# Performance work log

Measured on AMD Instinct MI355X. Metric: run time of the kernel, lower is better.

The kernel has to match this reference:

```python
import jax, jax.numpy as jnp
import numpy as np

B, S, D = 4, 2048, 1024
H, DK = 16, 64
NUM_BUCKETS = 32
MAX_DISTANCE = 128
EPS = 1e-6


def _relative_position_bucket(q_len, kv_len):
    # causal (bidirectional=False) T5 bucketization
    ctx = jnp.arange(q_len, dtype=jnp.int32)[:, None]
    mem = jnp.arange(kv_len, dtype=jnp.int32)[None, :]
    rp = mem - ctx                       # [q, kv]
    rp = -jnp.minimum(rp, 0)             # nonnegative distances to the past
    max_exact = NUM_BUCKETS // 2
    is_small = rp < max_exact
    rp_safe = jnp.maximum(rp, 1).astype(jnp.float32)
    large = max_exact + (
        jnp.log(rp_safe / max_exact) / np.log(MAX_DISTANCE / max_exact) * (NUM_BUCKETS - max_exact)
    ).astype(jnp.int32)
    large = jnp.minimum(large, NUM_BUCKETS - 1)
    return jnp.where(is_small, rp, large)  # [q, kv] int32 in [0, NUM_BUCKETS)


def setup_inputs() -> dict:
    key = jax.random.key(0)
    k1, k2, k3, k4 = jax.random.split(key, 4)
    hidden_states = jax.random.normal(k1, (B, S, D), dtype=jnp.float32)
    sequence_mask = jnp.ones((B, S), dtype=bool)
    rms_w = jnp.ones((D,), dtype=jnp.float32)
    W_qkv = jax.random.normal(k2, (D, 3 * H * DK), dtype=jnp.float32) * (D ** -0.5)
    W_o = jax.random.normal(k3, (H * DK, D), dtype=jnp.float32) * ((H * DK) ** -0.5)
    rel_bias = jax.random.normal(k4, (NUM_BUCKETS, H), dtype=jnp.float32)
    return {"hidden_states": hidden_states, "sequence_mask": sequence_mask,
            "rms_w": rms_w, "W_qkv": W_qkv, "W_o": W_o, "rel_bias": rel_bias}


def reference(hidden_states, sequence_mask, rms_w, W_qkv, W_o, rel_bias):
    # RMSNorm
    var = jnp.mean(hidden_states * hidden_states, axis=-1, keepdims=True)
    normed = hidden_states * jax.lax.rsqrt(var + EPS) * rms_w

    # QKV projection -> [B, S, 3, H, DK] -> [B, H, S, DK] each
    qkv = (normed @ W_qkv).reshape(B, S, 3, H, DK)
    q = jnp.transpose(qkv[:, :, 0], (0, 2, 1, 3))
    k = jnp.transpose(qkv[:, :, 1], (0, 2, 1, 3))
    v = jnp.transpose(qkv[:, :, 2], (0, 2, 1, 3))

    # relative position bias: gather [S,S,H] -> [1,H,S,S]
    bucket = _relative_position_bucket(S, S)
    pos_bias = jnp.transpose(rel_bias[bucket], (2, 0, 1))[None]

    # scores (note: T5 does NOT scale by 1/sqrt(dk))
    scores = jnp.einsum("bhqd,bhkd->bhqk", q, k) + pos_bias

    # causal mask combined with sequence mask (True = attend)
    causal = jnp.tril(jnp.ones((S, S), dtype=bool))
    mask = causal[None, None] & sequence_mask[:, None, None, :]
    scores = jnp.where(mask, scores, jnp.finfo(scores.dtype).min)

    attn = jax.nn.softmax(scores.astype(jnp.float32), axis=-1).astype(scores.dtype)
    # dropout p=0 / eval mode -> identity
    ctx = jnp.einsum("bhqk,bhkd->bhqd", attn, v)          # [B,H,S,DK]
    ctx = jnp.transpose(ctx, (0, 2, 1, 3)).reshape(B, S, H * DK)
    out = hidden_states + ctx @ W_o                        # residual
    return out
```

## Files before the change

kernel.cpp:

```cpp
#include <hip/hip_runtime.h>
#include <math.h>


typedef unsigned short ushort_t;
typedef __attribute__((ext_vector_type(8))) short bfrag;
typedef __attribute__((ext_vector_type(4))) float ffrag;

#define MFMA16(a, b, c) __builtin_amdgcn_mfma_f32_16x16x32_bf16((a), (b), (c), 0, 0, 0)
#define LOG2E 1.4426950408889634f

__device__ __forceinline__ void load_lds16(const ushort_t* g, ushort_t* l) {
  __builtin_amdgcn_global_load_lds(
      (const __attribute__((address_space(1))) unsigned int*)g,
      (__attribute__((address_space(3))) unsigned int*)l, 16, 0, 0);
}

__device__ __forceinline__ ushort_t f2bf(float f) {
  union { float f; unsigned u; } x; x.f = f;
  unsigned r = x.u + 0x7FFFu + ((x.u >> 16) & 1u);
  return (ushort_t)(r >> 16);
}
__device__ __forceinline__ float bf2f(ushort_t u) {
  union { unsigned u; float f; } x; x.u = ((unsigned)u) << 16; return x.f;
}
__device__ __forceinline__ unsigned cvtpk(float lo, float hi) {
  unsigned r;
  asm("v_cvt_pk_bf16_f32 %0, %1, %2" : "=v"(r) : "v"(lo), "v"(hi));
  return r;
}
__device__ __forceinline__ float exp2fast(float x) {
  return __builtin_amdgcn_exp2f(x);
}

__global__ __launch_bounds__(256) void norm_cvt_kernel(
    const float* __restrict__ hidden, const float* __restrict__ rms_w,
    ushort_t* __restrict__ normed) {
  const int w = threadIdx.x >> 6, lane = threadIdx.x & 63;
  const int row = blockIdx.x * 4 + w;
  const float* p = hidden + (size_t)row * 1024;
  float4 v[4];
  float s = 0.f;
#pragma unroll
  for (int i = 0; i < 4; ++i) {
    v[i] = *(const float4*)(p + (lane + i * 64) * 4);
    s += v[i].x * v[i].x + v[i].y * v[i].y + v[i].z * v[i].z + v[i].w * v[i].w;
  }
#pragma unroll
  for (int off = 1; off < 64; off <<= 1) s += __shfl_xor(s, off, 64);
  const float scale = rsqrtf(s * (1.0f / 1024.0f) + 1e-6f);
#pragma unroll
  for (int i = 0; i < 4; ++i) {
    const int c0 = (lane + i * 64) * 4;
    float4 wv = *(const float4*)(rms_w + c0);
    ushort4 u;
    u.x = f2bf(v[i].x * scale * wv.x);
    u.y = f2bf(v[i].y * scale * wv.y);
    u.z = f2bf(v[i].z * scale * wv.z);
    u.w = f2bf(v[i].w * scale * wv.w);
    *(ushort4*)(normed + (size_t)row * 1024 + c0) = u;
  }
}

__global__ __launch_bounds__(256) void transpose_cvt_kernel(
    const float* __restrict__ in, ushort_t* __restrict__ out, int R, int C) {
  __shared__ float tile[32][33];
  const int r0 = blockIdx.y * 32, c0 = blockIdx.x * 32;
  const int tr = threadIdx.x >> 5, tc = threadIdx.x & 31;
#pragma unroll
  for (int i = 0; i < 32; i += 8)
    tile[tr + i][tc] = in[(size_t)(r0 + tr + i) * C + c0 + tc];
  __syncthreads();
#pragma unroll
  for (int i = 0; i < 32; i += 8)
    out[(size_t)(c0 + tr + i) * R + r0 + tc] = f2bf(tile[tc][tr + i]);
}

__global__ __launch_bounds__(256, 2) void qkv_mfma_kernel(
    const ushort_t* __restrict__ A, const ushort_t* __restrict__ Bt,
    ushort_t* __restrict__ qbf, ushort_t* __restrict__ kbf,
    ushort_t* __restrict__ vtbf) {
  __shared__ ushort_t As[2][128][64];
  __shared__ ushort_t Bs[2][128][64];
  const int tid = threadIdx.x, lane = tid & 63, w = tid >> 6;
  const int quad = lane >> 4, ln = lane & 15;
  const int wr = w >> 1, wc = w & 1;
  const int id = blockIdx.x;
  const int xcd = id & 7, t8 = id >> 3;
  const int by = xcd * 8 + t8 / 24, bx = t8 % 24;
  const int m0 = by * 128, n0 = bx * 128;
  const int rswz = ln & 7;

  auto stage = [&](const ushort_t* src, ushort_t* lds, int gr0, int gc0) {
#pragma unroll
    for (int i = 0; i < 4; ++i) {
      const int idx = i * 256 + tid;
      const int r = idx >> 3, c = idx & 7;
      load_lds16(src + (size_t)(gr0 + r) * 1024 + gc0 + ((c ^ (r & 7)) * 8),
                 lds + idx * 8);
    }
  };

  ffrag acc[4][4];
#pragma unroll
  for (int i = 0; i < 4; ++i)
#pragma unroll
    for (int j = 0; j < 4; ++j) acc[i][j] = (ffrag)0.f;

  stage(A, &As[0][0][0], m0, 0);
  stage(Bt, &Bs[0][0][0], n0, 0);
  asm volatile("s_waitcnt vmcnt(0)" ::: "memory");
  __builtin_amdgcn_s_barrier();

  for (int t = 0; t < 16; ++t) {
    const int cur = t & 1;
    if (t + 1 < 16) {
      stage(A, &As[cur ^ 1][0][0], m0, (t + 1) * 64);
      stage(Bt, &Bs[cur ^ 1][0][0], n0, (t + 1) * 64);
    }
    bfrag a[4][2], b[4][2];
#pragma unroll
    for (int mi = 0; mi < 4; ++mi) {
      const int rA = wr * 64 + mi * 16 + ln;
#pragma unroll
      for (int ks = 0; ks < 2; ++ks)
        a[mi][ks] = *(const bfrag*)(&As[cur][rA][((ks * 4 + quad) ^ rswz) * 8]);
    }
#pragma unroll
    for (int ni = 0; ni < 4; ++ni) {
      const int rB = wc * 64 + ni * 16 + ln;
#pragma unroll
      for (int ks = 0; ks < 2; ++ks)
        b[ni][ks] = *(const bfrag*)(&Bs[cur][rB][((ks * 4 + quad) ^ rswz) * 8]);
    }
    __builtin_amdgcn_s_setprio(1);
#pragma unroll
    for (int mi = 0; mi < 4; ++mi)
#pragma unroll
      for (int ni = 0; ni < 4; ++ni)
#pragma unroll
        for (int ks = 0; ks < 2; ++ks)
          acc[mi][ni] = MFMA16(a[mi][ks], b[ni][ks], acc[mi][ni]);
    __builtin_amdgcn_s_setprio(0);
    asm volatile("s_waitcnt vmcnt(0)" ::: "memory");
    __builtin_amdgcn_s_barrier();
  }

  const int b_idx = m0 >> 11;
  const int cbase = n0 + wc * 64 + ln;
#pragma unroll
  for (int mi = 0; mi < 4; ++mi) {
    const int sbase = (m0 & 2047) + wr * 64 + mi * 16 + quad * 4;
#pragma unroll
    for (int ni = 0; ni < 4; ++ni) {
      const int c = cbase + ni * 16;
      const int three = c >> 10, rem = c & 1023;
      const int h = rem >> 6, dk = rem & 63;
      if (three == 2) {
        ushort4 u;
        u.x = f2bf(acc[mi][ni][0]); u.y = f2bf(acc[mi][ni][1]);
        u.z = f2bf(acc[mi][ni][2]); u.w = f2bf(acc[mi][ni][3]);
        *(ushort4*)(vtbf + ((size_t)(b_idx * 16 + h) * 64 + dk) * 2048 + sbase) = u;
      } else {
        const float sc = (three == 0) ? 1.0f : LOG2E;
        ushort_t* dst = (three == 0 ? qbf : kbf) +
                        ((size_t)(b_idx * 16 + h) * 2048 + sbase) * 64 + dk;
        dst[0]   = f2bf(acc[mi][ni][0] * sc);
        dst[64]  = f2bf(acc[mi][ni][1] * sc);
        dst[128] = f2bf(acc[mi][ni][2] * sc);
        dst[192] = f2bf(acc[mi][ni][3] * sc);
      }
    }
  }
}

__global__ __launch_bounds__(512, 6) void attn_mfma_kernel(
    const ushort_t* __restrict__ qbf, const ushort_t* __restrict__ kbf,
    const ushort_t* __restrict__ vtbf, const float* __restrict__ rel_bias,
    ushort_t* __restrict__ ctx) {
  __shared__ ushort_t Kt[2][2][64][32];
  __shared__ ushort_t Vt[2][2][64][32];
  __shared__ ushort_t Pt[128][64];
  __shared__ ushort_t bias_t[2048];

  const int tid = threadIdx.x, w = tid >> 6, lane = tid & 63;
  const int quad = lane >> 4, ln = lane & 15;
  const int id = blockIdx.x;
  const int bh = id & 63;
  const int qb = 15 - (id >> 6);
  const int h = bh & 15;
  const int nt = 2 * qb + 2;
  const int q0w = qb * 128 + w * 16;

  for (int dist = tid; dist < 2048; dist += 512) {
    int bucket;
    if (dist < 16) bucket = dist;
    else {
      bucket = 16 + (int)(logf((float)dist * (1.0f / 16.0f)) * (16.0f / logf(8.0f)));
      if (bucket > 31) bucket = 31;
    }
    bias_t[dist] = f2bf(rel_bias[bucket * 16 + h] * LOG2E);
  }
  const float c31 = bf2f(f2bf(rel_bias[31 * 16 + h] * LOG2E));
  __syncthreads();

  const size_t khead = (size_t)bh * 2048 * 64;
  const int skf = tid >> 8;
  const int srow = (tid >> 2) & 63;
  const int ssw = ((tid & 3) ^ ((srow >> 1) & 3)) * 8;
  const int rsw = ((ln >> 1) & 3) * 8;
  const int psw = (ln & 7) * 8;

  bfrag aq[2];
#pragma unroll
  for (int kf = 0; kf < 2; ++kf)
    aq[kf] = *(const bfrag*)(qbf + ((size_t)bh * 2048 + q0w + ln) * 64 +
                             kf * 32 + quad * 8);

  bfrag ones;
#pragma unroll
  for (int i = 0; i < 8; ++i) ones[i] = (short)0x3F80;

  ffrag o[4], l_acc;
#pragma unroll
  for (int nd = 0; nd < 4; ++nd) o[nd] = (ffrag)0.f;
  l_acc = (ffrag)0.f;
  float m_run = -3.0e38f;

  load_lds16(kbf + khead + (size_t)srow * 64 + skf * 32 + ssw,
             &Kt[0][0][0][0] + tid * 8);
  load_lds16(vtbf + khead + (size_t)srow * 2048 + 0 + skf * 32 + ssw,
             &Vt[0][0][0][0] + tid * 8);

  int cur = 0;
  for (int j = 0; j < nt; ++j) {
    const int key0 = j * 64;
    asm volatile("s_waitcnt vmcnt(0)" ::: "memory");
    __builtin_amdgcn_s_barrier();

    if (j + 1 < nt) {
      const int nk0 = key0 + 64;
      load_lds16(kbf + khead + (size_t)(nk0 + srow) * 64 + skf * 32 + ssw,
                 &Kt[cur ^ 1][0][0][0] + tid * 8);
      load_lds16(vtbf + khead + (size_t)srow * 2048 + nk0 + skf * 32 + ssw,
                 &Vt[cur ^ 1][0][0][0] + tid * 8);
    }

    if (key0 <= q0w + 15) {
      ffrag s[4];
#pragma unroll
      for (int mi = 0; mi < 4; ++mi) s[mi] = (ffrag)0.f;
      __builtin_amdgcn_s_setprio(1);
#pragma unroll
      for (int kf = 0; kf < 2; ++kf)
#pragma unroll
        for (int mi = 0; mi < 4; ++mi) {
          bfrag ak = *(const bfrag*)&Kt[cur][kf][mi * 16 + ln][(quad * 8) ^ rsw];
          s[mi] = MFMA16(ak, aq[kf], s[mi]);
        }
      __builtin_amdgcn_s_setprio(0);

      const bool diagT = (key0 + 63 > q0w);
      const bool fastT = (key0 + 176 <= q0w);
      float sbias = 0.f;
      if (fastT) {
        sbias = c31;
      } else if (diagT) {
        const int q = q0w + ln;
#pragma unroll
        for (int mi = 0; mi < 4; ++mi) {
          const int keyb = key0 + mi * 16 + quad * 4;
#pragma unroll
          for (int r = 0; r < 4; ++r) {
            const int dist = q - (keyb + r);
            const int db = dist < 0 ? 0 : dist;
            s[mi][r] = (dist < 0) ? -3.0e38f : (s[mi][r] + bf2f(bias_t[db]));
          }
        }
      } else {
        const int q = q0w + ln;
#pragma unroll
        for (int mi = 0; mi < 4; ++mi) {
          const int keyb = key0 + mi * 16 + quad * 4;
#pragma unroll
          for (int r = 0; r < 4; ++r)
            s[mi][r] += bf2f(bias_t[q - (keyb + r)]);
        }
      }

      float m0_ = fmaxf(fmaxf(s[0][0], s[0][1]), fmaxf(s[0][2], s[0][3]));
      float m1_ = fmaxf(fmaxf(s[1][0], s[1][1]), fmaxf(s[1][2], s[1][3]));
      float m2_ = fmaxf(fmaxf(s[2][0], s[2][1]), fmaxf(s[2][2], s[2][3]));
      float m3_ = fmaxf(fmaxf(s[3][0], s[3][1]), fmaxf(s[3][2], s[3][3]));
      const float mxl = fmaxf(fmaxf(m0_, m1_), fmaxf(m2_, m3_)) + sbias;

      if (!__all(mxl <= m_run + 8.0f)) {
        float mx = mxl;
        mx = fmaxf(mx, __shfl_xor(mx, 16, 64));
        mx = fmaxf(mx, __shfl_xor(mx, 32, 64));
        const float mnew = fmaxf(m_run, mx);
        const float alpha = exp2fast(m_run - mnew);
        m_run = mnew;
#pragma unroll
        for (int r = 0; r < 4; ++r) {
          const float af = __shfl(alpha, quad * 4 + r, 64);
#pragma unroll
          for (int nd = 0; nd < 4; ++nd) o[nd][r] *= af;
          l_acc[r] *= af;
        }
      }
      const float sh = m_run - sbias;
#pragma unroll
      for (int mi = 0; mi < 4; ++mi)
#pragma unroll
        for (int r = 0; r < 4; ++r)
          s[mi][r] = exp2fast(s[mi][r] - sh);

      {
        ushort_t* prow = &Pt[w * 16 + ln][0];
#pragma unroll
        for (int mi = 0; mi < 4; ++mi) {
          uint2 pk;
          pk.x = cvtpk(s[mi][0], s[mi][1]);
          pk.y = cvtpk(s[mi][2], s[mi][3]);
          *(uint2*)(prow + ((mi * 16 + quad * 4) ^ psw)) = pk;
        }
      }

      __builtin_amdgcn_s_setprio(1);
#pragma unroll
      for (int kf = 0; kf < 2; ++kf) {
        bfrag ap = *(const bfrag*)&Pt[w * 16 + ln][(kf * 32 + quad * 8) ^ psw];
        l_acc = MFMA16(ap, ones, l_acc);
#pragma unroll
        for (int nd = 0; nd < 4; ++nd) {
          bfrag bv = *(const bfrag*)&Vt[cur][kf][nd * 16 + ln][(quad * 8) ^ rsw];
          o[nd] = MFMA16(ap, bv, o[nd]);
        }
      }
      __builtin_amdgcn_s_setprio(0);
    }
    cur ^= 1;
  }

  ffrag inv;
#pragma unroll
  for (int r = 0; r < 4; ++r) inv[r] = 1.0f / l_acc[r];
  const int s0 = q0w + quad * 4;
#pragma unroll
  for (int nd = 0; nd < 4; ++nd)
#pragma unroll
    for (int r = 0; r < 4; ++r)
      ctx[((size_t)(bh >> 4) * 2048 + s0 + r) * 1024 + h * 64 + nd * 16 + ln] =
          f2bf(o[nd][r] * inv[r]);
}

__global__ __launch_bounds__(256, 2) void out_mfma_kernel(
    const ushort_t* __restrict__ A, const ushort_t* __restrict__ Bt,
    const float* __restrict__ hidden, float* __restrict__ out) {
  __shared__ ushort_t As[2][128][64];
  __shared__ ushort_t Bs[2][128][64];
  const int tid = threadIdx.x, lane = tid & 63, w = tid >> 6;
  const int quad = lane >> 4, ln = lane & 15;
  const int wr = w >> 1, wc = w & 1;
  const int id = blockIdx.x;
  const int xcd = id & 7, t = id >> 3;
  const int by = xcd * 8 + (t >> 3), bx = t & 7;
  const int m0 = by * 128, n0 = bx * 128;
  const int rswz = ln & 7;

  auto stage = [&](const ushort_t* src, ushort_t* lds, int gr0, int gc0) {
#pragma unroll
    for (int i = 0; i < 4; ++i) {
      const int idx = i * 256 + tid;
      const int r = idx >> 3, c = idx & 7;
      load_lds16(src + (size_t)(gr0 + r) * 1024 + gc0 + ((c ^ (r & 7)) * 8),
                 lds + idx * 8);
    }
  };

  ffrag acc[4][4];
#pragma unroll
  for (int i = 0; i < 4; ++i)
#pragma unroll
    for (int j = 0; j < 4; ++j) acc[i][j] = (ffrag)0.f;

  stage(A, &As[0][0][0], m0, 0);
  stage(Bt, &Bs[0][0][0], n0, 0);
  asm volatile("s_waitcnt vmcnt(0)" ::: "memory");
  __builtin_amdgcn_s_barrier();

  for (int t2 = 0; t2 < 16; ++t2) {
    const int cur = t2 & 1;
    if (t2 + 1 < 16) {
      stage(A, &As[cur ^ 1][0][0], m0, (t2 + 1) * 64);
      stage(Bt, &Bs[cur ^ 1][0][0], n0, (t2 + 1) * 64);
    }
    bfrag a[4][2], b[4][2];
#pragma unroll
    for (int mi = 0; mi < 4; ++mi) {
      const int rA = wr * 64 + mi * 16 + ln;
#pragma unroll
      for (int ks = 0; ks < 2; ++ks)
        a[mi][ks] = *(const bfrag*)(&As[cur][rA][((ks * 4 + quad) ^ rswz) * 8]);
    }
#pragma unroll
    for (int ni = 0; ni < 4; ++ni) {
      const int rB = wc * 64 + ni * 16 + ln;
#pragma unroll
      for (int ks = 0; ks < 2; ++ks)
        b[ni][ks] = *(const bfrag*)(&Bs[cur][rB][((ks * 4 + quad) ^ rswz) * 8]);
    }
    __builtin_amdgcn_s_setprio(1);
#pragma unroll
    for (int mi = 0; mi < 4; ++mi)
#pragma unroll
      for (int ni = 0; ni < 4; ++ni)
#pragma unroll
        for (int ks = 0; ks < 2; ++ks)
          acc[mi][ni] = MFMA16(a[mi][ks], b[ni][ks], acc[mi][ni]);
    __builtin_amdgcn_s_setprio(0);
    asm volatile("s_waitcnt vmcnt(0)" ::: "memory");
    __builtin_amdgcn_s_barrier();
  }

#pragma unroll
  for (int mi = 0; mi < 4; ++mi) {
    const int m = m0 + wr * 64 + mi * 16 + quad * 4;
#pragma unroll
    for (int ni = 0; ni < 4; ++ni) {
      const int c = n0 + wc * 64 + ni * 16 + ln;
#pragma unroll
      for (int r = 0; r < 4; ++r) {
        const size_t off = (size_t)(m + r) * 1024 + c;
        out[off] = acc[mi][ni][r] + hidden[off];
      }
    }
  }
}

extern "C" void kernel_launch(void* const* d_in, const int* in_sizes, int n_in,
                              void* d_out, int out_size, void* d_ws, size_t ws_size,
                              hipStream_t stream) {
  const size_t NORMED = (size_t)8192 * 1024;
  const size_t WQKVT  = (size_t)3072 * 1024;
  const size_t WOT    = (size_t)1024 * 1024;
  const size_t QKVE   = (size_t)64 * 2048 * 64;
  const size_t need = (NORMED + WQKVT + WOT + 3 * QKVE + NORMED) * 2;
  if (ws_size < need) return;

  const float* hidden   = (const float*)d_in[0];
  const float* rms_w    = (const float*)d_in[2];
  const float* Wqkv     = (const float*)d_in[3];
  const float* Wo       = (const float*)d_in[4];
  const float* rel_bias = (const float*)d_in[5];
  float* out = (float*)d_out;

  ushort_t* normed = (ushort_t*)d_ws;
  ushort_t* wqkvt  = normed + NORMED;
  ushort_t* wot    = wqkvt + WQKVT;
  ushort_t* qbf    = wot + WOT;
  ushort_t* kbf    = qbf + QKVE;
  ushort_t* vtbf   = kbf + QKVE;
  ushort_t* ctx    = vtbf + QKVE;

  norm_cvt_kernel<<<2048, 256, 0, stream>>>(hidden, rms_w, normed);
  transpose_cvt_kernel<<<dim3(96, 32), 256, 0, stream>>>(Wqkv, wqkvt, 1024, 3072);
  transpose_cvt_kernel<<<dim3(32, 32), 256, 0, stream>>>(Wo, wot, 1024, 1024);
  qkv_mfma_kernel<<<1536, 256, 0, stream>>>(normed, wqkvt, qbf, kbf, vtbf);
  attn_mfma_kernel<<<1024, 512, 0, stream>>>(qbf, kbf, vtbf, rel_bias, ctx);
  out_mfma_kernel<<<512, 256, 0, stream>>>(ctx, wot, hidden, out);
}
```

Measured before the change: 258.7 us.

## Give each attention wave two query sub-tiles and halve block threads

The attention kernel now runs 256 threads (4 waves) per block, and each wave handles 32 query rows as two 16-row sub-tiles instead of 16 rows. Each K and V fragment read from LDS is reused across both sub-tiles, which halves LDS traffic per MFMA and amortises the K/V staging over fewer waves. Each thread now issues two global-to-LDS loads per buffer. The cost is twice the accumulator and score registers per wave, hence the lower occupancy target (3 blocks of 256 threads instead of 6 blocks of 512), and fewer waves are left to hide latency.

```diff
diff --git a/kernel.cpp b/kernel.cpp
--- a/kernel.cpp
+++ b/kernel.cpp
@@ -173,7 +173,7 @@
   }
 }
 
-__global__ __launch_bounds__(512, 6) void attn_mfma_kernel(
+__global__ __launch_bounds__(256, 3) void attn_mfma_kernel(
     const ushort_t* __restrict__ qbf, const ushort_t* __restrict__ kbf,
     const ushort_t* __restrict__ vtbf, const float* __restrict__ rel_bias,
     ushort_t* __restrict__ ctx) {
@@ -189,9 +189,9 @@
   const int qb = 15 - (id >> 6);
   const int h = bh & 15;
   const int nt = 2 * qb + 2;
-  const int q0w = qb * 128 + w * 16;
-
-  for (int dist = tid; dist < 2048; dist += 512) {
+  const int q0w = qb * 128 + w * 32;
+
+  for (int dist = tid; dist < 2048; dist += 256) {
     int bucket;
     if (dist < 16) bucket = dist;
     else {
@@ -204,32 +204,44 @@
   __syncthreads();
 
   const size_t khead = (size_t)bh * 2048 * 64;
-  const int skf = tid >> 8;
-  const int srow = (tid >> 2) & 63;
-  const int ssw = ((tid & 3) ^ ((srow >> 1) & 3)) * 8;
   const int rsw = ((ln >> 1) & 3) * 8;
   const int psw = (ln & 7) * 8;
 
-  bfrag aq[2];
-#pragma unroll
-  for (int kf = 0; kf < 2; ++kf)
-    aq[kf] = *(const bfrag*)(qbf + ((size_t)bh * 2048 + q0w + ln) * 64 +
-                             kf * 32 + quad * 8);
+  bfrag aq[2][2];
+#pragma unroll
+  for (int ni = 0; ni < 2; ++ni)
+#pragma unroll
+    for (int kf = 0; kf < 2; ++kf)
+      aq[ni][kf] = *(const bfrag*)(qbf + ((size_t)bh * 2048 + q0w + ni * 16 + ln) * 64 +
+                                   kf * 32 + quad * 8);
 
   bfrag ones;
 #pragma unroll
   for (int i = 0; i < 8; ++i) ones[i] = (short)0x3F80;
 
-  ffrag o[4], l_acc;
-#pragma unroll
-  for (int nd = 0; nd < 4; ++nd) o[nd] = (ffrag)0.f;
-  l_acc = (ffrag)0.f;
-  float m_run = -3.0e38f;
-
-  load_lds16(kbf + khead + (size_t)srow * 64 + skf * 32 + ssw,
-             &Kt[0][0][0][0] + tid * 8);
-  load_lds16(vtbf + khead + (size_t)srow * 2048 + 0 + skf * 32 + ssw,
-             &Vt[0][0][0][0] + tid * 8);
+  ffrag o[2][4], l_acc[2];
+#pragma unroll
+  for (int mo = 0; mo < 2; ++mo) {
+#pragma unroll
+    for (int nd = 0; nd < 4; ++nd) o[mo][nd] = (ffrag)0.f;
+    l_acc[mo] = (ffrag)0.f;
+  }
+  float m_run[2] = {-3.0e38f, -3.0e38f};
+
+  auto stageKV = [&](int key0, int buf) {
+#pragma unroll
+    for (int i = 0; i < 2; ++i) {
+      const int cid = i * 256 + tid;
+      const int kf = cid >> 8, row = (cid >> 2) & 63, c8 = cid & 3;
+      const int sw = (c8 ^ ((row >> 1) & 3)) * 8;
+      load_lds16(kbf + khead + (size_t)(key0 + row) * 64 + kf * 32 + sw,
+                 &Kt[buf][0][0][0] + cid * 8);
+      load_lds16(vtbf + khead + (size_t)row * 2048 + key0 + kf * 32 + sw,
+                 &Vt[buf][0][0][0] + cid * 8);
+    }
+  };
+
+  stageKV(0, 0);
 
   int cur = 0;
   for (int j = 0; j < nt; ++j) {
@@ -237,91 +249,103 @@
     asm volatile("s_waitcnt vmcnt(0)" ::: "memory");
     __builtin_amdgcn_s_barrier();
 
-    if (j + 1 < nt) {
-      const int nk0 = key0 + 64;
-      load_lds16(kbf + khead + (size_t)(nk0 + srow) * 64 + skf * 32 + ssw,
-                 &Kt[cur ^ 1][0][0][0] + tid * 8);
-      load_lds16(vtbf + khead + (size_t)srow * 2048 + nk0 + skf * 32 + ssw,
-                 &Vt[cur ^ 1][0][0][0] + tid * 8);
-    }
-
-    if (key0 <= q0w + 15) {
-      ffrag s[4];
-#pragma unroll
-      for (int mi = 0; mi < 4; ++mi) s[mi] = (ffrag)0.f;
+    if (j + 1 < nt) stageKV(key0 + 64, cur ^ 1);
+
+    if (key0 <= q0w + 31) {
+      ffrag s[4][2];
+#pragma unroll
+      for (int mi = 0; mi < 4; ++mi)
+#pragma unroll
+        for (int ni = 0; ni < 2; ++ni) s[mi][ni] = (ffrag)0.f;
       __builtin_amdgcn_s_setprio(1);
 #pragma unroll
       for (int kf = 0; kf < 2; ++kf)
 #pragma unroll
         for (int mi = 0; mi < 4; ++mi) {
           bfrag ak = *(const bfrag*)&Kt[cur][kf][mi * 16 + ln][(quad * 8) ^ rsw];
-          s[mi] = MFMA16(ak, aq[kf], s[mi]);
+          s[mi][0] = MFMA16(ak, aq[0][kf], s[mi][0]);
+          s[mi][1] = MFMA16(ak, aq[1][kf], s[mi][1]);
         }
       __builtin_amdgcn_s_setprio(0);
 
-      const bool diagT = (key0 + 63 > q0w);
       const bool fastT = (key0 + 176 <= q0w);
       float sbias = 0.f;
       if (fastT) {
         sbias = c31;
-      } else if (diagT) {
-        const int q = q0w + ln;
-#pragma unroll
-        for (int mi = 0; mi < 4; ++mi) {
-          const int keyb = key0 + mi * 16 + quad * 4;
-#pragma unroll
-          for (int r = 0; r < 4; ++r) {
-            const int dist = q - (keyb + r);
-            const int db = dist < 0 ? 0 : dist;
-            s[mi][r] = (dist < 0) ? -3.0e38f : (s[mi][r] + bf2f(bias_t[db]));
+      } else {
+#pragma unroll
+        for (int ni = 0; ni < 2; ++ni) {
+          const int q = q0w + ni * 16 + ln;
+          if (key0 + 63 > q0w + ni * 16) {
+#pragma unroll
+            for (int mi = 0; mi < 4; ++mi) {
+              const int keyb = key0 + mi * 16 + quad * 4;
+#pragma unroll
+              for (int r = 0; r < 4; ++r) {
+                const int dist = q - (keyb + r);
+                const int db = dist < 0 ? 0 : dist;
+                s[mi][ni][r] = (dist < 0) ? -3.0e38f
+                                          : (s[mi][ni][r] + bf2f(bias_t[db]));
+              }
+            }
+          } else {
+#pragma unroll
+            for (int mi = 0; mi < 4; ++mi) {
+              const int keyb = key0 + mi * 16 + quad * 4;
+#pragma unroll
+              for (int r = 0; r < 4; ++r)
+                s[mi][ni][r] += bf2f(bias_t[q - (keyb + r)]);
+            }
           }
         }
-      } else {
-        const int q = q0w + ln;
-#pragma unroll
-        for (int mi = 0; mi < 4; ++mi) {
-          const int keyb = key0 + mi * 16 + quad * 4;
+      }
+
+      float mxl[2];
+#pragma unroll
+      for (int ni = 0; ni < 2; ++ni) {
+        float a0 = fmaxf(fmaxf(s[0][ni][0], s[0][ni][1]), fmaxf(s[0][ni][2], s[0][ni][3]));
+        float a1 = fmaxf(fmaxf(s[1][ni][0], s[1][ni][1]), fmaxf(s[1][ni][2], s[1][ni][3]));
+        float a2 = fmaxf(fmaxf(s[2][ni][0], s[2][ni][1]), fmaxf(s[2][ni][2], s[2][ni][3]));
+        float a3 = fmaxf(fmaxf(s[3][ni][0], s[3][ni][1]), fmaxf(s[3][ni][2], s[3][ni][3]));
+        mxl[ni] = fmaxf(fmaxf(a0, a1), fmaxf(a2, a3)) + sbias;
+      }
+
+      if (!__all(mxl[0] <= m_run[0] + 8.0f && mxl[1] <= m_run[1] + 8.0f)) {
+#pragma unroll
+        for (int ni = 0; ni < 2; ++ni) {
+          float mx = mxl[ni];
+          mx = fmaxf(mx, __shfl_xor(mx, 16, 64));
+          mx = fmaxf(mx, __shfl_xor(mx, 32, 64));
+          const float mnew = fmaxf(m_run[ni], mx);
+          const float alpha = exp2fast(m_run[ni] - mnew);
+          m_run[ni] = mnew;
+#pragma unroll
+          for (int r = 0; r < 4; ++r) {
+            const float af = __shfl(alpha, quad * 4 + r, 64);
+#pragma unroll
+            for (int nd = 0; nd < 4; ++nd) o[ni][nd][r] *= af;
+            l_acc[ni][r] *= af;
+          }
+        }
+      }
+#pragma unroll
+      for (int ni = 0; ni < 2; ++ni) {
+        const float sh = m_run[ni] - sbias;
+#pragma unroll
+        for (int mi = 0; mi < 4; ++mi)
 #pragma unroll
           for (int r = 0; r < 4; ++r)
-            s[mi][r] += bf2f(bias_t[q - (keyb + r)]);
-        }
-      }
-
-      float m0_ = fmaxf(fmaxf(s[0][0], s[0][1]), fmaxf(s[0][2], s[0][3]));
-      float m1_ = fmaxf(fmaxf(s[1][0], s[1][1]), fmaxf(s[1][2], s[1][3]));
-      float m2_ = fmaxf(fmaxf(s[2][0], s[2][1]), fmaxf(s[2][2], s[2][3]));
-      float m3_ = fmaxf(fmaxf(s[3][0], s[3][1]), fmaxf(s[3][2], s[3][3]));
-      const float mxl = fmaxf(fmaxf(m0_, m1_), fmaxf(m2_, m3_)) + sbias;
-
-      if (!__all(mxl <= m_run + 8.0f)) {
-        float mx = mxl;
-        mx = fmaxf(mx, __shfl_xor(mx, 16, 64));
-        mx = fmaxf(mx, __shfl_xor(mx, 32, 64));
-        const float mnew = fmaxf(m_run, mx);
-        const float alpha = exp2fast(m_run - mnew);
-        m_run = mnew;
-#pragma unroll
-        for (int r = 0; r < 4; ++r) {
-          const float af = __shfl(alpha, quad * 4 + r, 64);
-#pragma unroll
-          for (int nd = 0; nd < 4; ++nd) o[nd][r] *= af;
-          l_acc[r] *= af;
-        }
-      }
-      const float sh = m_run - sbias;
-#pragma unroll
-      for (int mi = 0; mi < 4; ++mi)
-#pragma unroll
-        for (int r = 0; r < 4; ++r)
-          s[mi][r] = exp2fast(s[mi][r] - sh);
-
-      {
-        ushort_t* prow = &Pt[w * 16 + ln][0];
+            s[mi][ni][r] = exp2fast(s[mi][ni][r] - sh);
+      }
+
+#pragma unroll
+      for (int ni = 0; ni < 2; ++ni) {
+        ushort_t* prow = &Pt[w * 32 + ni * 16 + ln][0];
 #pragma unroll
         for (int mi = 0; mi < 4; ++mi) {
           uint2 pk;
-          pk.x = cvtpk(s[mi][0], s[mi][1]);
-          pk.y = cvtpk(s[mi][2], s[mi][3]);
+          pk.x = cvtpk(s[mi][ni][0], s[mi][ni][1]);
+          pk.y = cvtpk(s[mi][ni][2], s[mi][ni][3]);
           *(uint2*)(prow + ((mi * 16 + quad * 4) ^ psw)) = pk;
         }
       }
@@ -329,12 +353,15 @@
       __builtin_amdgcn_s_setprio(1);
 #pragma unroll
       for (int kf = 0; kf < 2; ++kf) {
-        bfrag ap = *(const bfrag*)&Pt[w * 16 + ln][(kf * 32 + quad * 8) ^ psw];
-        l_acc = MFMA16(ap, ones, l_acc);
+        bfrag ap0 = *(const bfrag*)&Pt[w * 32 + ln][(kf * 32 + quad * 8) ^ psw];
+        bfrag ap1 = *(const bfrag*)&Pt[w * 32 + 16 + ln][(kf * 32 + quad * 8) ^ psw];
+        l_acc[0] = MFMA16(ap0, ones, l_acc[0]);
+        l_acc[1] = MFMA16(ap1, ones, l_acc[1]);
 #pragma unroll
         for (int nd = 0; nd < 4; ++nd) {
           bfrag bv = *(const bfrag*)&Vt[cur][kf][nd * 16 + ln][(quad * 8) ^ rsw];
-          o[nd] = MFMA16(ap, bv, o[nd]);
+          o[0][nd] = MFMA16(ap0, bv, o[0][nd]);
+          o[1][nd] = MFMA16(ap1, bv, o[1][nd]);
         }
       }
       __builtin_amdgcn_s_setprio(0);
@@ -342,16 +369,19 @@
     cur ^= 1;
   }
 
-  ffrag inv;
-#pragma unroll
-  for (int r = 0; r < 4; ++r) inv[r] = 1.0f / l_acc[r];
-  const int s0 = q0w + quad * 4;
-#pragma unroll
-  for (int nd = 0; nd < 4; ++nd)
-#pragma unroll
-    for (int r = 0; r < 4; ++r)
-      ctx[((size_t)(bh >> 4) * 2048 + s0 + r) * 1024 + h * 64 + nd * 16 + ln] =
-          f2bf(o[nd][r] * inv[r]);
+#pragma unroll
+  for (int mo = 0; mo < 2; ++mo) {
+    ffrag inv;
+#pragma unroll
+    for (int r = 0; r < 4; ++r) inv[r] = 1.0f / l_acc[mo][r];
+    const int s0 = q0w + mo * 16 + quad * 4;
+#pragma unroll
+    for (int nd = 0; nd < 4; ++nd)
+#pragma unroll
+      for (int r = 0; r < 4; ++r)
+        ctx[((size_t)(bh >> 4) * 2048 + s0 + r) * 1024 + h * 64 + nd * 16 + ln] =
+            f2bf(o[mo][nd][r] * inv[r]);
+  }
 }
 
 __global__ __launch_bounds__(256, 2) void out_mfma_kernel(
@@ -467,6 +497,6 @@
   transpose_cvt_kernel<<<dim3(96, 32), 256, 0, stream>>>(Wqkv, wqkvt, 1024, 3072);
   transpose_cvt_kernel<<<dim3(32, 32), 256, 0, stream>>>(Wo, wot, 1024, 1024);
   qkv_mfma_kernel<<<1536, 256, 0, stream>>>(normed, wqkvt, qbf, kbf, vtbf);
-  attn_mfma_kernel<<<1024, 512, 0, stream>>>(qbf, kbf, vtbf, rel_bias, ctx);
+  attn_mfma_kernel<<<1024, 256, 0, stream>>>(qbf, kbf, vtbf, rel_bias, ctx);
   out_mfma_kernel<<<512, 256, 0, stream>>>(ctx, wot, hidden, out);
 }
```

After: 258.6 us. No clear change (-0.0%).
